# Optimization experiments

Hardware: AMD Instinct MI355X
Metric: run time of the kernel (lower is better)

The kernel has to match this reference:

```python
import jax, jax.numpy as jnp
import numpy as np

B, S, D, H = 8, 8192, 256, 256


def setup_inputs() -> dict:
    key = jax.random.key(0)
    ks = jax.random.split(key, 5)
    scale = 1.0 / np.sqrt(D)  # mimic nn.Linear init scale
    return {
        "x": jax.random.normal(ks[0], (B, S, D), dtype=jnp.float32),
        "h0": jnp.zeros((B, 1, H), dtype=jnp.float32),
        "w_h_w": jax.random.normal(ks[1], (H, D), dtype=jnp.float32) * scale,
        "w_h_b": jax.random.normal(ks[2], (H,), dtype=jnp.float32) * scale,
        "w_z_w": jax.random.normal(ks[3], (H, D), dtype=jnp.float32) * scale,
        "w_z_b": jax.random.normal(ks[4], (H,), dtype=jnp.float32) * scale,
    }


def reference(x, h0, w_h_w, w_h_b, w_z_w, w_z_b):
    # Projections over the whole sequence (same math as per-step Linear calls)
    z = jax.nn.sigmoid(jnp.einsum('bsd,hd->bsh', x, w_z_w) + w_z_b)  # [B,S,H]
    h_tilde = jnp.einsum('bsd,hd->bsh', x, w_h_w) + w_h_b            # [B,S,H]

    def step(h_prev, zh):
        z_t, ht_t = zh  # each [B,H]
        h_t = (1.0 - z_t) * h_prev + z_t * ht_t
        return h_t, h_t

    # scan over time axis; carry is [B,H]
    _, hs = jax.lax.scan(step, h0[:, 0],
                         (jnp.swapaxes(z, 0, 1), jnp.swapaxes(h_tilde, 0, 1)))
    return jnp.swapaxes(hs, 0, 1)  # [B,S,H]
```

## Files before the change

### kernel.cpp

```cpp
#include <hip/hip_runtime.h>
#include <math.h>


constexpr int B_ = 8;
constexpr int S_ = 8192;
constexpr int D_ = 256;
constexpr int H_ = 256;
constexpr int M_ = B_ * S_;
constexpr int CHUNKS = 128;
constexpr int CLEN = S_ / CHUNKS;

typedef __attribute__((ext_vector_type(8))) short bf16x8;
typedef __attribute__((ext_vector_type(4))) float f32x4;

__device__ __forceinline__ uint pack2bf(float f0, float f1) {
  const uint u0 = __float_as_uint(f0) + 0x8000u;
  const uint u1 = __float_as_uint(f1) + 0x8000u;
  return __builtin_amdgcn_perm(u1, u0, 0x07060302u);
}

union SMem {
  struct {
    ushort xs[128][72];
    ushort wzs[64][72];
    ushort whs[64][72];
  } s;
  uint abt[128][66];
};

__global__ __launch_bounds__(256) void gemm_zh(
    const float* __restrict__ x,
    const float* __restrict__ whw, const float* __restrict__ whb,
    const float* __restrict__ wzw, const float* __restrict__ wzb,
    uint* __restrict__ ab,
    float* __restrict__ P_out, float* __restrict__ Q_out)
{
  __shared__ SMem sm;

  const int tid = threadIdx.x;
  const int g    = blockIdx.x;
  const int xcd  = g & 7;
  const int loc  = g >> 3;
  const int nt   = loc & 3;
  const int panel = (loc >> 2) * 8 + xcd;
  const int m0 = panel * 128;
  const int n0 = nt * 64;

  const int lane = tid & 63;
  const int w  = tid >> 6;
  const int mb = (w & 1) * 64;
  const int nb = (w >> 1) * 32;
  const int q  = lane >> 4;
  const int cn = lane & 15;

  f32x4 accz[4][2] = {};
  f32x4 acch[4][2] = {};

  for (int k0 = 0; k0 < D_; k0 += 64) {
    __syncthreads();
#pragma unroll
    for (int f = 0; f < 8; f++) {
      const int idx = tid + 256 * f;
      const int row = idx >> 4, seg = idx & 15;
      float4 v = *(const float4*)(x + (size_t)(m0 + row) * D_ + k0 + seg * 4);
      *(uint2*)&sm.s.xs[row][seg * 4] =
          make_uint2(pack2bf(v.x, v.y), pack2bf(v.z, v.w));
    }
#pragma unroll
    for (int f = 0; f < 4; f++) {
      const int idx = tid + 256 * f;
      const int row = idx >> 4, seg = idx & 15;
      float4 vz = *(const float4*)(wzw + (size_t)(n0 + row) * D_ + k0 + seg * 4);
      float4 vh = *(const float4*)(whw + (size_t)(n0 + row) * D_ + k0 + seg * 4);
      *(uint2*)&sm.s.wzs[row][seg * 4] =
          make_uint2(pack2bf(vz.x, vz.y), pack2bf(vz.z, vz.w));
      *(uint2*)&sm.s.whs[row][seg * 4] =
          make_uint2(pack2bf(vh.x, vh.y), pack2bf(vh.z, vh.w));
    }
    __syncthreads();
#pragma unroll
    for (int ks = 0; ks < 2; ks++) {
      const int kk = ks * 32 + q * 8;
      bf16x8 af[4], bz[2], bh[2];
#pragma unroll
      for (int i = 0; i < 4; i++)
        af[i] = *(const bf16x8*)&sm.s.xs[mb + i * 16 + cn][kk];
#pragma unroll
      for (int j = 0; j < 2; j++) {
        bz[j] = *(const bf16x8*)&sm.s.wzs[nb + j * 16 + cn][kk];
        bh[j] = *(const bf16x8*)&sm.s.whs[nb + j * 16 + cn][kk];
      }
#pragma unroll
      for (int i = 0; i < 4; i++)
#pragma unroll
        for (int j = 0; j < 2; j++) {
          accz[i][j] = __builtin_amdgcn_mfma_f32_16x16x32_bf16(af[i], bz[j], accz[i][j], 0, 0, 0);
          acch[i][j] = __builtin_amdgcn_mfma_f32_16x16x32_bf16(af[i], bh[j], acch[i][j], 0, 0, 0);
        }
    }
  }

  __syncthreads();

#pragma unroll
  for (int j = 0; j < 2; j++) {
    const int chl = nb + j * 16 + cn;
    const int ch = n0 + chl;
    const float zb = wzb[ch], hb = whb[ch];
#pragma unroll
    for (int i = 0; i < 4; i++) {
#pragma unroll
      for (int r = 0; r < 4; r++) {
        const int rowl = mb + i * 16 + q * 4 + r;
        const float zpre = accz[i][j][r] + zb;
        const float hpre = acch[i][j][r] + hb;
        const float zs = 1.0f / (1.0f + __expf(-zpre));
        const uint packed = pack2bf(1.0f - zs, zs * hpre);
        ab[(size_t)(m0 + rowl) * H_ + ch] = packed;
        sm.abt[rowl][chl] = packed;
      }
    }
  }

  __syncthreads();

  if (tid < 128) {
    const int k = tid >> 6;
    const int chl = tid & 63;
    float P = 1.0f, Q = 0.0f;
#pragma unroll 8
    for (int t = 0; t < CLEN; t++) {
      const uint v = sm.abt[k * 64 + t][chl];
      const float a = __uint_as_float(v << 16);
      const float b = __uint_as_float(v & 0xFFFF0000u);
      Q = fmaf(a, Q, b);
      P *= a;
    }
    const int bidx = m0 / S_;
    const int cglob = (m0 % S_) / CLEN + k;
    const size_t idx = ((size_t)bidx * CHUNKS + cglob) * H_ + n0 + chl;
    P_out[idx] = P;
    Q_out[idx] = Q;
  }
}

__global__ __launch_bounds__(256) void scan_phaseB(
    const float* __restrict__ h0in, const float* __restrict__ P,
    const float* __restrict__ Q, float* __restrict__ hstate)
{
  const int b = blockIdx.x;
  const int h = threadIdx.x;
  const size_t base = (size_t)b * CHUNKS * H_ + h;
  float hc = h0in[(size_t)b * H_ + h];
  for (int c0 = 0; c0 < CHUNKS; c0 += 8) {
    float p[8], q[8];
#pragma unroll
    for (int j = 0; j < 8; j++) {
      p[j] = P[base + (size_t)(c0 + j) * H_];
      q[j] = Q[base + (size_t)(c0 + j) * H_];
    }
#pragma unroll
    for (int j = 0; j < 8; j++) {
      hstate[base + (size_t)(c0 + j) * H_] = hc;
      hc = fmaf(p[j], hc, q[j]);
    }
  }
}

__global__ __launch_bounds__(256) void scan_phaseC(
    const uint* __restrict__ ab, const float* __restrict__ hstate,
    float* __restrict__ out)
{
  const int pair = blockIdx.x * 4 + (threadIdx.x >> 6);
  const int b = pair >> 7;
  const int c = pair & 127;
  const int ch = (threadIdx.x & 63) * 4;
  const size_t base = ((size_t)b * S_ + (size_t)c * CLEN) * H_ + ch;
  float4 h = *(const float4*)(hstate + ((size_t)b * CHUNKS + c) * H_ + ch);
  for (int t0 = 0; t0 < CLEN; t0 += 8) {
    uint4 v[8];
#pragma unroll
    for (int j = 0; j < 8; j++)
      v[j] = *(const uint4*)(ab + base + (size_t)(t0 + j) * H_);
#pragma unroll
    for (int j = 0; j < 8; j++) {
      h.x = fmaf(__uint_as_float(v[j].x << 16), h.x, __uint_as_float(v[j].x & 0xFFFF0000u));
      h.y = fmaf(__uint_as_float(v[j].y << 16), h.y, __uint_as_float(v[j].y & 0xFFFF0000u));
      h.z = fmaf(__uint_as_float(v[j].z << 16), h.z, __uint_as_float(v[j].z & 0xFFFF0000u));
      h.w = fmaf(__uint_as_float(v[j].w << 16), h.w, __uint_as_float(v[j].w & 0xFFFF0000u));
      *(float4*)(out + base + (size_t)(t0 + j) * H_) = h;
    }
  }
}

extern "C" void kernel_launch(void* const* d_in, const int* in_sizes, int n_in,
                              void* d_out, int out_size, void* d_ws, size_t ws_size,
                              hipStream_t stream) {
  const float* x   = (const float*)d_in[0];
  const float* h0  = (const float*)d_in[1];
  const float* whw = (const float*)d_in[2];
  const float* whb = (const float*)d_in[3];
  const float* wzw = (const float*)d_in[4];
  const float* wzb = (const float*)d_in[5];
  float* out = (float*)d_out;

  uint*  ab     = (uint*)d_ws;
  float* chunkP = (float*)(ab + (size_t)M_ * H_);
  float* chunkQ = chunkP + (size_t)B_ * CHUNKS * H_;
  float* hstate = chunkQ + (size_t)B_ * CHUNKS * H_;

  gemm_zh<<<(M_ / 128) * 4, 256, 0, stream>>>(x, whw, whb, wzw, wzb,
                                              ab, chunkP, chunkQ);
  scan_phaseB<<<B_, 256, 0, stream>>>(h0, chunkP, chunkQ, hstate);
  scan_phaseC<<<(B_ * CHUNKS) / 4, 256, 0, stream>>>(ab, hstate, out);
}
```

Baseline: 196.8 us.

## Fuse GEMM and chunked scan into one kernel with decoupled look-back

Replaces the three-kernel pipeline (GEMM writing a bf16 ab buffer, serial chunk-carry scan, per-chunk replay) with a single kernel. Each block computes the projections for one 64-step chunk across all 256 channels, loading fragments straight from global memory without LDS staging. It keeps the gate/candidate pair in LDS and resolves the inter-chunk carry with flag-based decoupled look-back before writing outputs. This removes the global round trip of the intermediate ab tensor and two launches. In exchange it relies on forward-progress assumptions for spin-waiting blocks, adds a memset, and recomputes weight fragment loads per block without shared-memory reuse.

```diff
diff --git a/kernel.cpp b/kernel.cpp
--- a/kernel.cpp
+++ b/kernel.cpp
@@ -6,9 +6,9 @@
 constexpr int S_ = 8192;
 constexpr int D_ = 256;
 constexpr int H_ = 256;
-constexpr int M_ = B_ * S_;
 constexpr int CHUNKS = 128;
-constexpr int CLEN = S_ / CHUNKS;
+constexpr int CLEN = 64;
+constexpr int NBLK = B_ * CHUNKS;
 
 typedef __attribute__((ext_vector_type(8))) short bf16x8;
 typedef __attribute__((ext_vector_type(4))) float f32x4;
@@ -19,176 +19,190 @@
   return __builtin_amdgcn_perm(u1, u0, 0x07060302u);
 }
 
-union SMem {
-  struct {
-    ushort xs[128][72];
-    ushort wzs[64][72];
-    ushort whs[64][72];
-  } s;
-  uint abt[128][66];
-};
-
-__global__ __launch_bounds__(256) void gemm_zh(
-    const float* __restrict__ x,
+__device__ __forceinline__ bf16x8 pack8(float4 lo, float4 hi) {
+  union { uint4 u; bf16x8 v; } r;
+  r.u = make_uint4(pack2bf(lo.x, lo.y), pack2bf(lo.z, lo.w),
+                   pack2bf(hi.x, hi.y), pack2bf(hi.z, hi.w));
+  return r.v;
+}
+
+__device__ __forceinline__ float4 fma4(float4 a, float4 x, float4 b) {
+  return make_float4(fmaf(a.x, x.x, b.x), fmaf(a.y, x.y, b.y),
+                     fmaf(a.z, x.z, b.z), fmaf(a.w, x.w, b.w));
+}
+__device__ __forceinline__ float4 mul4(float4 a, float4 b) {
+  return make_float4(a.x * b.x, a.y * b.y, a.z * b.z, a.w * b.w);
+}
+
+__global__ __launch_bounds__(256, 2) void mingru_mega(
+    const float* __restrict__ x, const float* __restrict__ h0,
     const float* __restrict__ whw, const float* __restrict__ whb,
     const float* __restrict__ wzw, const float* __restrict__ wzb,
-    uint* __restrict__ ab,
-    float* __restrict__ P_out, float* __restrict__ Q_out)
+    float* __restrict__ out,
+    float* __restrict__ chunkP, float* __restrict__ chunkQ,
+    float* __restrict__ chunkH, uint* __restrict__ flags)
 {
-  __shared__ SMem sm;
-
+  __shared__ uint abt[CLEN][260];
+  __shared__ float4 segP[4][64];
+  __shared__ float4 segQ[4][64];
+  __shared__ float4 hin4[64];
+
+  const int bid = blockIdx.x;
+  const int b = bid >> 7;
+  const int c = bid & 127;
   const int tid = threadIdx.x;
-  const int g    = blockIdx.x;
-  const int xcd  = g & 7;
-  const int loc  = g >> 3;
-  const int nt   = loc & 3;
-  const int panel = (loc >> 2) * 8 + xcd;
-  const int m0 = panel * 128;
-  const int n0 = nt * 64;
-
+  const int w = tid >> 6;
   const int lane = tid & 63;
-  const int w  = tid >> 6;
-  const int mb = (w & 1) * 64;
-  const int nb = (w >> 1) * 32;
-  const int q  = lane >> 4;
   const int cn = lane & 15;
-
-  f32x4 accz[4][2] = {};
-  f32x4 acch[4][2] = {};
-
-  for (int k0 = 0; k0 < D_; k0 += 64) {
-    __syncthreads();
-#pragma unroll
-    for (int f = 0; f < 8; f++) {
-      const int idx = tid + 256 * f;
-      const int row = idx >> 4, seg = idx & 15;
-      float4 v = *(const float4*)(x + (size_t)(m0 + row) * D_ + k0 + seg * 4);
-      *(uint2*)&sm.s.xs[row][seg * 4] =
-          make_uint2(pack2bf(v.x, v.y), pack2bf(v.z, v.w));
-    }
-#pragma unroll
-    for (int f = 0; f < 4; f++) {
-      const int idx = tid + 256 * f;
-      const int row = idx >> 4, seg = idx & 15;
-      float4 vz = *(const float4*)(wzw + (size_t)(n0 + row) * D_ + k0 + seg * 4);
-      float4 vh = *(const float4*)(whw + (size_t)(n0 + row) * D_ + k0 + seg * 4);
-      *(uint2*)&sm.s.wzs[row][seg * 4] =
-          make_uint2(pack2bf(vz.x, vz.y), pack2bf(vz.z, vz.w));
-      *(uint2*)&sm.s.whs[row][seg * 4] =
-          make_uint2(pack2bf(vh.x, vh.y), pack2bf(vh.z, vh.w));
-    }
-    __syncthreads();
-#pragma unroll
-    for (int ks = 0; ks < 2; ks++) {
-      const int kk = ks * 32 + q * 8;
-      bf16x8 af[4], bz[2], bh[2];
+  const int q = lane >> 4;
+  const int chw = w * 64;
+  const size_t rowbase = (size_t)b * S_ + (size_t)c * CLEN;
+
+  f32x4 accz[4][4] = {};
+  f32x4 acch[4][4] = {};
+
+  const float* xp  = x   + (rowbase + cn) * D_ + q * 8;
+  const float* wzp = wzw + (size_t)(chw + cn) * D_ + q * 8;
+  const float* whp = whw + (size_t)(chw + cn) * D_ + q * 8;
+
+#pragma unroll 2
+  for (int kk = 0; kk < D_; kk += 32) {
+    bf16x8 af[4];
+#pragma unroll
+    for (int i = 0; i < 4; i++) {
+      const float* p = xp + i * 16 * D_ + kk;
+      af[i] = pack8(*(const float4*)p, *(const float4*)(p + 4));
+    }
+    {
+      bf16x8 bz[4];
+#pragma unroll
+      for (int j = 0; j < 4; j++) {
+        const float* p = wzp + j * 16 * D_ + kk;
+        bz[j] = pack8(*(const float4*)p, *(const float4*)(p + 4));
+      }
 #pragma unroll
       for (int i = 0; i < 4; i++)
-        af[i] = *(const bf16x8*)&sm.s.xs[mb + i * 16 + cn][kk];
-#pragma unroll
-      for (int j = 0; j < 2; j++) {
-        bz[j] = *(const bf16x8*)&sm.s.wzs[nb + j * 16 + cn][kk];
-        bh[j] = *(const bf16x8*)&sm.s.whs[nb + j * 16 + cn][kk];
+#pragma unroll
+        for (int j = 0; j < 4; j++)
+          accz[i][j] = __builtin_amdgcn_mfma_f32_16x16x32_bf16(
+              af[i], bz[j], accz[i][j], 0, 0, 0);
+    }
+    {
+      bf16x8 bh[4];
+#pragma unroll
+      for (int j = 0; j < 4; j++) {
+        const float* p = whp + j * 16 * D_ + kk;
+        bh[j] = pack8(*(const float4*)p, *(const float4*)(p + 4));
       }
 #pragma unroll
       for (int i = 0; i < 4; i++)
 #pragma unroll
-        for (int j = 0; j < 2; j++) {
-          accz[i][j] = __builtin_amdgcn_mfma_f32_16x16x32_bf16(af[i], bz[j], accz[i][j], 0, 0, 0);
-          acch[i][j] = __builtin_amdgcn_mfma_f32_16x16x32_bf16(af[i], bh[j], acch[i][j], 0, 0, 0);
-        }
-    }
-  }
-
-  __syncthreads();
-
-#pragma unroll
-  for (int j = 0; j < 2; j++) {
-    const int chl = nb + j * 16 + cn;
-    const int ch = n0 + chl;
+        for (int j = 0; j < 4; j++)
+          acch[i][j] = __builtin_amdgcn_mfma_f32_16x16x32_bf16(
+              af[i], bh[j], acch[i][j], 0, 0, 0);
+    }
+  }
+
+#pragma unroll
+  for (int j = 0; j < 4; j++) {
+    const int ch = chw + j * 16 + cn;
     const float zb = wzb[ch], hb = whb[ch];
 #pragma unroll
     for (int i = 0; i < 4; i++) {
 #pragma unroll
       for (int r = 0; r < 4; r++) {
-        const int rowl = mb + i * 16 + q * 4 + r;
+        const int row = i * 16 + q * 4 + r;
         const float zpre = accz[i][j][r] + zb;
         const float hpre = acch[i][j][r] + hb;
-        const float zs = 1.0f / (1.0f + __expf(-zpre));
-        const uint packed = pack2bf(1.0f - zs, zs * hpre);
-        ab[(size_t)(m0 + rowl) * H_ + ch] = packed;
-        sm.abt[rowl][chl] = packed;
-      }
-    }
-  }
-
+        const float e = __expf(-zpre);
+        const float rcp = __builtin_amdgcn_rcpf(1.0f + e);
+        abt[row][ch] = pack2bf(e * rcp, hpre * rcp);
+      }
+    }
+  }
   __syncthreads();
 
-  if (tid < 128) {
-    const int k = tid >> 6;
-    const int chl = tid & 63;
-    float P = 1.0f, Q = 0.0f;
-#pragma unroll 8
-    for (int t = 0; t < CLEN; t++) {
-      const uint v = sm.abt[k * 64 + t][chl];
-      const float a = __uint_as_float(v << 16);
-      const float b = __uint_as_float(v & 0xFFFF0000u);
-      Q = fmaf(a, Q, b);
-      P *= a;
-    }
-    const int bidx = m0 / S_;
-    const int cglob = (m0 % S_) / CLEN + k;
-    const size_t idx = ((size_t)bidx * CHUNKS + cglob) * H_ + n0 + chl;
-    P_out[idx] = P;
-    Q_out[idx] = Q;
-  }
-}
-
-__global__ __launch_bounds__(256) void scan_phaseB(
-    const float* __restrict__ h0in, const float* __restrict__ P,
-    const float* __restrict__ Q, float* __restrict__ hstate)
-{
-  const int b = blockIdx.x;
-  const int h = threadIdx.x;
-  const size_t base = (size_t)b * CHUNKS * H_ + h;
-  float hc = h0in[(size_t)b * H_ + h];
-  for (int c0 = 0; c0 < CHUNKS; c0 += 8) {
-    float p[8], q[8];
-#pragma unroll
-    for (int j = 0; j < 8; j++) {
-      p[j] = P[base + (size_t)(c0 + j) * H_];
-      q[j] = Q[base + (size_t)(c0 + j) * H_];
-    }
-#pragma unroll
-    for (int j = 0; j < 8; j++) {
-      hstate[base + (size_t)(c0 + j) * H_] = hc;
-      hc = fmaf(p[j], hc, q[j]);
-    }
-  }
-}
-
-__global__ __launch_bounds__(256) void scan_phaseC(
-    const uint* __restrict__ ab, const float* __restrict__ hstate,
-    float* __restrict__ out)
-{
-  const int pair = blockIdx.x * 4 + (threadIdx.x >> 6);
-  const int b = pair >> 7;
-  const int c = pair & 127;
-  const int ch = (threadIdx.x & 63) * 4;
-  const size_t base = ((size_t)b * S_ + (size_t)c * CLEN) * H_ + ch;
-  float4 h = *(const float4*)(hstate + ((size_t)b * CHUNKS + c) * H_ + ch);
-  for (int t0 = 0; t0 < CLEN; t0 += 8) {
-    uint4 v[8];
-#pragma unroll
-    for (int j = 0; j < 8; j++)
-      v[j] = *(const uint4*)(ab + base + (size_t)(t0 + j) * H_);
-#pragma unroll
-    for (int j = 0; j < 8; j++) {
-      h.x = fmaf(__uint_as_float(v[j].x << 16), h.x, __uint_as_float(v[j].x & 0xFFFF0000u));
-      h.y = fmaf(__uint_as_float(v[j].y << 16), h.y, __uint_as_float(v[j].y & 0xFFFF0000u));
-      h.z = fmaf(__uint_as_float(v[j].z << 16), h.z, __uint_as_float(v[j].z & 0xFFFF0000u));
-      h.w = fmaf(__uint_as_float(v[j].w << 16), h.w, __uint_as_float(v[j].w & 0xFFFF0000u));
-      *(float4*)(out + base + (size_t)(t0 + j) * H_) = h;
+  {
+    float4 P = make_float4(1.f, 1.f, 1.f, 1.f);
+    float4 Q = make_float4(0.f, 0.f, 0.f, 0.f);
+#pragma unroll
+    for (int t = 0; t < 16; t++) {
+      const uint4 v = *(const uint4*)&abt[w * 16 + t][lane * 4];
+      const float4 a = make_float4(__uint_as_float(v.x << 16), __uint_as_float(v.y << 16),
+                                   __uint_as_float(v.z << 16), __uint_as_float(v.w << 16));
+      const float4 bb = make_float4(__uint_as_float(v.x & 0xFFFF0000u), __uint_as_float(v.y & 0xFFFF0000u),
+                                    __uint_as_float(v.z & 0xFFFF0000u), __uint_as_float(v.w & 0xFFFF0000u));
+      Q = fma4(a, Q, bb);
+      P = mul4(P, a);
+    }
+    segP[w][lane] = P;
+    segQ[w][lane] = Q;
+  }
+  __syncthreads();
+
+  if (tid < 64) {
+    float4 Pb = segP[0][lane], Qb = segQ[0][lane];
+#pragma unroll
+    for (int s = 1; s < 4; s++) {
+      const float4 Ps = segP[s][lane], Qs = segQ[s][lane];
+      Qb = fma4(Ps, Qb, Qs);
+      Pb = mul4(Pb, Ps);
+    }
+    const size_t cb = (size_t)bid * H_ + lane * 4;
+    float4 hinv;
+    if (c == 0) {
+      hinv = *(const float4*)(h0 + (size_t)b * H_ + lane * 4);
+    } else {
+      *(float4*)(chunkP + cb) = Pb;
+      *(float4*)(chunkQ + cb) = Qb;
+      __hip_atomic_store(&flags[bid], 1u, __ATOMIC_RELEASE,
+                         __HIP_MEMORY_SCOPE_AGENT);
+      float4 Pa = make_float4(1.f, 1.f, 1.f, 1.f);
+      float4 Qa = make_float4(0.f, 0.f, 0.f, 0.f);
+      int j = c - 1;
+      for (;;) {
+        const uint f = __hip_atomic_load(&flags[b * CHUNKS + j],
+                                         __ATOMIC_ACQUIRE,
+                                         __HIP_MEMORY_SCOPE_AGENT);
+        if (__all(f >= 2u)) {
+          const float4 Hj = *(const float4*)(chunkH + (size_t)(b * CHUNKS + j) * H_ + lane * 4);
+          hinv = fma4(Pa, Hj, Qa);
+          break;
+        } else if (__all(f >= 1u)) {
+          const float4 Pj = *(const float4*)(chunkP + (size_t)(b * CHUNKS + j) * H_ + lane * 4);
+          const float4 Qj = *(const float4*)(chunkQ + (size_t)(b * CHUNKS + j) * H_ + lane * 4);
+          Qa = fma4(Pa, Qj, Qa);
+          Pa = mul4(Pa, Pj);
+          --j;
+        } else {
+          __builtin_amdgcn_s_sleep(4);
+        }
+      }
+    }
+    *(float4*)(chunkH + cb) = fma4(Pb, hinv, Qb);
+    __hip_atomic_store(&flags[bid], 2u, __ATOMIC_RELEASE,
+                       __HIP_MEMORY_SCOPE_AGENT);
+    hin4[lane] = hinv;
+  }
+  __syncthreads();
+
+  {
+    float4 st = hin4[lane];
+#pragma unroll
+    for (int s = 0; s < 3; s++)
+      if (s < w) {
+        st = fma4(segP[s][lane], st, segQ[s][lane]);
+      }
+    float* op = out + (rowbase + w * 16) * H_ + lane * 4;
+#pragma unroll
+    for (int t = 0; t < 16; t++) {
+      const uint4 v = *(const uint4*)&abt[w * 16 + t][lane * 4];
+      const float4 a = make_float4(__uint_as_float(v.x << 16), __uint_as_float(v.y << 16),
+                                   __uint_as_float(v.z << 16), __uint_as_float(v.w << 16));
+      const float4 bb = make_float4(__uint_as_float(v.x & 0xFFFF0000u), __uint_as_float(v.y & 0xFFFF0000u),
+                                    __uint_as_float(v.z & 0xFFFF0000u), __uint_as_float(v.w & 0xFFFF0000u));
+      st = fma4(a, st, bb);
+      *(float4*)(op + (size_t)t * H_) = st;
     }
   }
 }
@@ -204,13 +218,12 @@
   const float* wzb = (const float*)d_in[5];
   float* out = (float*)d_out;
 
-  uint*  ab     = (uint*)d_ws;
-  float* chunkP = (float*)(ab + (size_t)M_ * H_);
-  float* chunkQ = chunkP + (size_t)B_ * CHUNKS * H_;
-  float* hstate = chunkQ + (size_t)B_ * CHUNKS * H_;
-
-  gemm_zh<<<(M_ / 128) * 4, 256, 0, stream>>>(x, whw, whb, wzw, wzb,
-                                              ab, chunkP, chunkQ);
-  scan_phaseB<<<B_, 256, 0, stream>>>(h0, chunkP, chunkQ, hstate);
-  scan_phaseC<<<(B_ * CHUNKS) / 4, 256, 0, stream>>>(ab, hstate, out);
-}
+  float* chunkP = (float*)d_ws;
+  float* chunkQ = chunkP + (size_t)NBLK * H_;
+  float* chunkH = chunkQ + (size_t)NBLK * H_;
+  uint*  flags  = (uint*)(chunkH + (size_t)NBLK * H_);
+
+  hipMemsetAsync(flags, 0, NBLK * sizeof(uint), stream);
+  mingru_mega<<<NBLK, 256, 0, stream>>>(x, h0, whw, whb, wzw, wzb, out,
+                                        chunkP, chunkQ, chunkH, flags);
+}
```

New measurement: 371.9 us. +89.0%, slower.
